# Kernel tuning notes

Measured on AMD Instinct MI355X. Metric: run time of the kernel, lower is better.

The kernel has to match this reference:

```python
import jax, jax.numpy as jnp
import numpy as np

B, C, L, H, W = 4, 96, 32, 56, 56
KD = 16
NUM_SCALES = 2  # 1 + ceil(log2(L / KD)) for L=32, KD=16


def setup_inputs() -> dict:
    key = jax.random.key(0)
    ks = jax.random.split(key, 5)
    x = jax.random.normal(ks[0], (B, C, L, H, W), jnp.float32)
    width_conv = jax.random.normal(ks[1], (C, W), jnp.float32)
    height_conv = jax.random.normal(ks[2], (C, H), jnp.float32)
    kernel0 = jax.random.normal(ks[3], (1, C, KD), jnp.float32)
    kernel1 = jax.random.normal(ks[4], (1, C, KD), jnp.float32)
    # decay init: rand*(decay_max-decay_min)+decay_min == 2.0 exactly (min==max==2)
    decay = jnp.full((1, C, 1), 2.0, jnp.float32)
    return dict(x=x, width_conv=width_conv, height_conv=height_conv,
                kernel0=kernel0, kernel1=kernel1, decay=decay)


def _interp_linear(k, scale):
    """F.interpolate(k, scale_factor=scale, mode='linear', align_corners=False)."""
    if scale == 1:
        return k
    Lk = k.shape[-1]
    out_len = Lk * scale
    src = jnp.maximum((jnp.arange(out_len, dtype=jnp.float32) + 0.5) / scale - 0.5, 0.0)
    lo = jnp.floor(src).astype(jnp.int32)
    frac = src - lo.astype(jnp.float32)
    hi = jnp.minimum(lo + 1, Lk - 1)
    return k[..., lo] * (1.0 - frac) + k[..., hi] * frac


def _fftconv(x, kf, axis, n, out_len):
    # causal FFT conv with zero-padding to n=2*dim, truncated back to out_len
    xf = jnp.fft.rfft(x, n=n, axis=axis)
    y = jnp.fft.irfft(xf * kf, n=n, axis=axis)
    return jax.lax.slice_in_dim(y, 0, out_len, axis=axis)


def _length_kernel(kernel0, kernel1, decay):
    parts = []
    for i, kern in enumerate((kernel0, kernel1)):
        ki = _interp_linear(kern, 2 ** i) * decay ** (NUM_SCALES - i - 1)
        parts.append(ki)
    k = jnp.concatenate(parts, axis=-1)[0, :, :L]            # (C, L)
    norm = jax.lax.stop_gradient(jnp.linalg.norm(k, axis=-1, keepdims=True))
    return k / norm


def reference(x, width_conv, height_conv, kernel0, kernel1, decay):
    # x: (B, C, L, H, W). The torch rearranges are pure layout moves; the math is
    # a per-channel 1D FFT conv along W, then H, then L.
    kf_w = jnp.fft.rfft(width_conv, n=2 * W)                 # (C, W+1)
    x = _fftconv(x, kf_w[None, :, None, None, :], axis=4, n=2 * W, out_len=W)
    kf_h = jnp.fft.rfft(height_conv, n=2 * H)                # (C, H+1)
    x = _fftconv(x, kf_h[None, :, None, :, None], axis=3, n=2 * H, out_len=H)
    k = _length_kernel(kernel0, kernel1, decay)              # (C, L)
    kf_l = jnp.fft.rfft(k, n=2 * L)                          # (C, L+1)
    x = _fftconv(x, kf_l[None, :, :, None, None], axis=2, n=2 * L, out_len=L)
    return x
```

## Files before the change

### kernel.cpp

```cpp
#include <hip/hip_runtime.h>

#define BB 4
#define CC 96
#define LL 32
#define HH 56
#define WW 56
#define HW (HH * WW)
#define KD 16
#define CH 14

__global__ __launch_bounds__(256, 3) void conv_wh(const float* __restrict__ x,
                                                  const float* __restrict__ wconv,
                                                  const float* __restrict__ hconv,
                                                  float* __restrict__ out) {
    __shared__ float sl[4][HH][WW + 1];

    const int tid  = threadIdx.x;
    const int wv   = tid >> 6;
    const int lane = tid & 63;
    const int slice0 = blockIdx.x * 4;
    const int c      = (slice0 / LL) % CC;
    const float* __restrict__ kw = wconv + c * WW;
    const float* __restrict__ kh = hconv + c * HH;

    const size_t base = (size_t)(slice0 + wv) * HW;
    #pragma unroll
    for (int i = 0; i < HW / 64; ++i) {
        int m = i * 64 + lane;
        sl[wv][m / WW][m % WW] = x[base + m];
    }
    __syncthreads();

    if (lane < HH) {
        float* row = &sl[wv][lane][0];
        #pragma unroll
        for (int t = 3; t >= 0; --t) {
            const int w0 = t * CH;
            float acc[CH];
            #pragma unroll
            for (int i = 0; i < CH; ++i) acc[i] = 0.f;
            #pragma unroll
            for (int u = 0; u < t; ++u) {
                const int u0 = u * CH;
                float xch[CH];
                #pragma unroll
                for (int j = 0; j < CH; ++j) xch[j] = row[u0 + j];
                #pragma unroll
                for (int dd = 0; dd < 2 * CH - 1; ++dd) {
                    const float kd = kw[w0 - u0 - (CH - 1) + dd];
                    const int delta = dd - (CH - 1);
                    #pragma unroll
                    for (int j = 0; j < CH; ++j) {
                        const int i = j + delta;
                        if (i >= 0 && i < CH)
                            acc[i] = fmaf(kd, xch[j], acc[i]);
                    }
                }
            }
            {
                float xch[CH];
                #pragma unroll
                for (int j = 0; j < CH; ++j) xch[j] = row[w0 + j];
                #pragma unroll
                for (int dd = 0; dd < CH; ++dd) {
                    const float kd = kw[dd];
                    #pragma unroll
                    for (int j = 0; j < CH - dd; ++j)
                        acc[j + dd] = fmaf(kd, xch[j], acc[j + dd]);
                }
            }
            #pragma unroll
            for (int i = 0; i < CH; ++i) row[w0 + i] = acc[i];
        }
    }
    __syncthreads();

    if (lane < WW) {
        #pragma unroll
        for (int t = 3; t >= 0; --t) {
            const int h0 = t * CH;
            float acc[CH];
            #pragma unroll
            for (int i = 0; i < CH; ++i) acc[i] = 0.f;
            #pragma unroll
            for (int u = 0; u < t; ++u) {
                const int u0 = u * CH;
                float xch[CH];
                #pragma unroll
                for (int j = 0; j < CH; ++j) xch[j] = sl[wv][u0 + j][lane];
                #pragma unroll
                for (int dd = 0; dd < 2 * CH - 1; ++dd) {
                    const float kd = kh[h0 - u0 - (CH - 1) + dd];
                    const int delta = dd - (CH - 1);
                    #pragma unroll
                    for (int j = 0; j < CH; ++j) {
                        const int i = j + delta;
                        if (i >= 0 && i < CH)
                            acc[i] = fmaf(kd, xch[j], acc[i]);
                    }
                }
            }
            {
                float xch[CH];
                #pragma unroll
                for (int j = 0; j < CH; ++j) xch[j] = sl[wv][h0 + j][lane];
                #pragma unroll
                for (int dd = 0; dd < CH; ++dd) {
                    const float kd = kh[dd];
                    #pragma unroll
                    for (int j = 0; j < CH - dd; ++j)
                        acc[j + dd] = fmaf(kd, xch[j], acc[j + dd]);
                }
            }
            #pragma unroll
            for (int i = 0; i < CH; ++i)
                out[base + (size_t)(h0 + i) * WW + lane] = acc[i];
        }
    }
}

__global__ __launch_bounds__(256, 2) void conv_l(float* __restrict__ y,
                                                 const float* __restrict__ k0,
                                                 const float* __restrict__ k1,
                                                 const float* __restrict__ decay) {
    __shared__ float kl[LL];
    __shared__ float s_norm;

    const int tid = threadIdx.x;
    const int bc  = blockIdx.y;
    const int c   = bc % CC;

    if (tid < LL) {
        float v;
        const float dec = decay[c];
        if (tid < KD) {
            v = k0[c * KD + tid] * dec;
        } else {
            const int   i    = tid - KD;
            const float src  = fmaxf((i + 0.5f) * 0.5f - 0.5f, 0.f);
            const int   lo   = (int)floorf(src);
            const float frac = src - (float)lo;
            const int   hi   = min(lo + 1, KD - 1);
            v = k1[c * KD + lo] * (1.f - frac) + k1[c * KD + hi] * frac;
        }
        kl[tid] = v;
    }
    __syncthreads();
    if (tid == 0) {
        float s = 0.f;
        for (int i = 0; i < LL; ++i) s += kl[i] * kl[i];
        s_norm = sqrtf(s);
    }
    __syncthreads();

    const float inv = 1.0f / s_norm;
    float kr[LL];
    #pragma unroll
    for (int i = 0; i < LL; ++i) kr[i] = kl[i] * inv;

    const int pos = blockIdx.x * 256 + tid;
    if (pos >= HW) return;

    float* col = y + (size_t)bc * LL * HW + pos;
    float xin[LL];
    #pragma unroll
    for (int l = 0; l < LL; ++l) xin[l] = col[(size_t)l * HW];

    #pragma unroll
    for (int l = LL - 1; l >= 0; --l) {
        float t = 0.f;
        #pragma unroll
        for (int j = 0; j <= l; ++j)
            t = fmaf(kr[l - j], xin[j], t);
        xin[l] = t;
    }
    #pragma unroll
    for (int l = 0; l < LL; ++l) col[(size_t)l * HW] = xin[l];
}

extern "C" void kernel_launch(void* const* d_in, const int* in_sizes, int n_in,
                              void* d_out, int out_size, void* d_ws, size_t ws_size,
                              hipStream_t stream) {
    const float* x     = (const float*)d_in[0];
    const float* wconv = (const float*)d_in[1];
    const float* hconv = (const float*)d_in[2];
    const float* k0    = (const float*)d_in[3];
    const float* k1    = (const float*)d_in[4];
    const float* dec   = (const float*)d_in[5];
    float*       out   = (float*)d_out;

    conv_wh<<<dim3(BB * CC * LL / 4), 256, 0, stream>>>(x, wconv, hconv, out);
    conv_l<<<dim3((HW + 255) / 256, BB * CC), 256, 0, stream>>>(out, k0, k1, dec);
}
```

Baseline: 342.2 us.

## Store W/H conv tiles as packed bf16 in LDS and vectorize L conv

The W/H convolution kernel now stores its shared-memory slice as packed bf16 pairs instead of fp32. This halves LDS use, and the launch-bounds occupancy target rises from 3 to 6 blocks. Global loads become float2. The L-axis kernel processes two adjacent spatial positions per thread with float2 loads and stores and drops its launch bounds. Rounding intermediates to bf16 lowers numerical accuracy compared with the fp32 reference and may break tolerance.

Result: slower. 476.8 us (+39.3%).

```diff
diff --git a/kernel.cpp b/kernel.cpp
--- a/kernel.cpp
+++ b/kernel.cpp
@@ -9,11 +9,21 @@
 #define KD 16
 #define CH 14
 
-__global__ __launch_bounds__(256, 3) void conv_wh(const float* __restrict__ x,
+__device__ __forceinline__ unsigned rne16(float f) {
+    unsigned u = __float_as_uint(f);
+    return u + 0x7fffu + ((u >> 16) & 1u);
+}
+__device__ __forceinline__ unsigned packbf(float a, float b) {
+    return (rne16(a) >> 16) | (rne16(b) & 0xffff0000u);
+}
+__device__ __forceinline__ float lo16(unsigned u) { return __uint_as_float(u << 16); }
+__device__ __forceinline__ float hi16(unsigned u) { return __uint_as_float(u & 0xffff0000u); }
+
+__global__ __launch_bounds__(256, 6) void conv_wh(const float* __restrict__ x,
                                                   const float* __restrict__ wconv,
                                                   const float* __restrict__ hconv,
                                                   float* __restrict__ out) {
-    __shared__ float sl[4][HH][WW + 1];
+    __shared__ unsigned slu[4][HH][29];
 
     const int tid  = threadIdx.x;
     const int wv   = tid >> 6;
@@ -24,15 +34,19 @@
     const float* __restrict__ kh = hconv + c * HH;
 
     const size_t base = (size_t)(slice0 + wv) * HW;
-    #pragma unroll
-    for (int i = 0; i < HW / 64; ++i) {
-        int m = i * 64 + lane;
-        sl[wv][m / WW][m % WW] = x[base + m];
+    const float2* xs = (const float2*)(x + base);
+    #pragma unroll
+    for (int i = 0; i < 25; ++i) {
+        int d = i * 64 + lane;
+        if (d < HW / 2) {
+            float2 v = xs[d];
+            slu[wv][d / 28][d % 28] = packbf(v.x, v.y);
+        }
     }
     __syncthreads();
 
     if (lane < HH) {
-        float* row = &sl[wv][lane][0];
+        unsigned* rowp = &slu[wv][lane][0];
         #pragma unroll
         for (int t = 3; t >= 0; --t) {
             const int w0 = t * CH;
@@ -44,7 +58,11 @@
                 const int u0 = u * CH;
                 float xch[CH];
                 #pragma unroll
-                for (int j = 0; j < CH; ++j) xch[j] = row[u0 + j];
+                for (int jj = 0; jj < CH / 2; ++jj) {
+                    unsigned v = rowp[7 * u + jj];
+                    xch[2 * jj]     = lo16(v);
+                    xch[2 * jj + 1] = hi16(v);
+                }
                 #pragma unroll
                 for (int dd = 0; dd < 2 * CH - 1; ++dd) {
                     const float kd = kw[w0 - u0 - (CH - 1) + dd];
@@ -60,7 +78,11 @@
             {
                 float xch[CH];
                 #pragma unroll
-                for (int j = 0; j < CH; ++j) xch[j] = row[w0 + j];
+                for (int jj = 0; jj < CH / 2; ++jj) {
+                    unsigned v = rowp[7 * t + jj];
+                    xch[2 * jj]     = lo16(v);
+                    xch[2 * jj + 1] = hi16(v);
+                }
                 #pragma unroll
                 for (int dd = 0; dd < CH; ++dd) {
                     const float kd = kw[dd];
@@ -70,12 +92,15 @@
                 }
             }
             #pragma unroll
-            for (int i = 0; i < CH; ++i) row[w0 + i] = acc[i];
+            for (int jj = 0; jj < CH / 2; ++jj)
+                rowp[7 * t + jj] = packbf(acc[2 * jj], acc[2 * jj + 1]);
         }
     }
     __syncthreads();
 
     if (lane < WW) {
+        const int wq  = lane >> 1;
+        const bool od = lane & 1;
         #pragma unroll
         for (int t = 3; t >= 0; --t) {
             const int h0 = t * CH;
@@ -87,7 +112,10 @@
                 const int u0 = u * CH;
                 float xch[CH];
                 #pragma unroll
-                for (int j = 0; j < CH; ++j) xch[j] = sl[wv][u0 + j][lane];
+                for (int j = 0; j < CH; ++j) {
+                    unsigned v = slu[wv][u0 + j][wq];
+                    xch[j] = od ? hi16(v) : lo16(v);
+                }
                 #pragma unroll
                 for (int dd = 0; dd < 2 * CH - 1; ++dd) {
                     const float kd = kh[h0 - u0 - (CH - 1) + dd];
@@ -103,7 +131,10 @@
             {
                 float xch[CH];
                 #pragma unroll
-                for (int j = 0; j < CH; ++j) xch[j] = sl[wv][h0 + j][lane];
+                for (int j = 0; j < CH; ++j) {
+                    unsigned v = slu[wv][h0 + j][wq];
+                    xch[j] = od ? hi16(v) : lo16(v);
+                }
                 #pragma unroll
                 for (int dd = 0; dd < CH; ++dd) {
                     const float kd = kh[dd];
@@ -119,10 +150,10 @@
     }
 }
 
-__global__ __launch_bounds__(256, 2) void conv_l(float* __restrict__ y,
-                                                 const float* __restrict__ k0,
-                                                 const float* __restrict__ k1,
-                                                 const float* __restrict__ decay) {
+__global__ void conv_l(float* __restrict__ y,
+                       const float* __restrict__ k0,
+                       const float* __restrict__ k1,
+                       const float* __restrict__ decay) {
     __shared__ float kl[LL];
     __shared__ float s_norm;
 
@@ -158,24 +189,26 @@
     #pragma unroll
     for (int i = 0; i < LL; ++i) kr[i] = kl[i] * inv;
 
-    const int pos = blockIdx.x * 256 + tid;
-    if (pos >= HW) return;
-
-    float* col = y + (size_t)bc * LL * HW + pos;
-    float xin[LL];
-    #pragma unroll
-    for (int l = 0; l < LL; ++l) xin[l] = col[(size_t)l * HW];
+    const int pos2 = blockIdx.x * 256 + tid;
+    if (pos2 >= HW / 2) return;
+
+    float2* col = (float2*)(y + (size_t)bc * LL * HW) + pos2;
+    float2 xin[LL];
+    #pragma unroll
+    for (int l = 0; l < LL; ++l) xin[l] = col[(size_t)l * (HW / 2)];
 
     #pragma unroll
     for (int l = LL - 1; l >= 0; --l) {
-        float t = 0.f;
+        float tx = 0.f, ty = 0.f;
         #pragma unroll
-        for (int j = 0; j <= l; ++j)
-            t = fmaf(kr[l - j], xin[j], t);
-        xin[l] = t;
-    }
-    #pragma unroll
-    for (int l = 0; l < LL; ++l) col[(size_t)l * HW] = xin[l];
+        for (int j = 0; j <= l; ++j) {
+            tx = fmaf(kr[l - j], xin[j].x, tx);
+            ty = fmaf(kr[l - j], xin[j].y, ty);
+        }
+        xin[l].x = tx; xin[l].y = ty;
+    }
+    #pragma unroll
+    for (int l = 0; l < LL; ++l) col[(size_t)l * (HW / 2)] = xin[l];
 }
 
 extern "C" void kernel_launch(void* const* d_in, const int* in_sizes, int n_in,
@@ -190,5 +223,5 @@
     float*       out   = (float*)d_out;
 
     conv_wh<<<dim3(BB * CC * LL / 4), 256, 0, stream>>>(x, wconv, hconv, out);
-    conv_l<<<dim3((HW + 255) / 256, BB * CC), 256, 0, stream>>>(out, k0, k1, dec);
-}
+    conv_l<<<dim3((HW / 2 + 255) / 256, BB * CC), 256, 0, stream>>>(out, k0, k1, dec);
+}
```
